# Kernel tuning notes

Hardware: AMD Instinct MI355X
Metric: run time of the kernel (lower is better)

The kernel has to match this reference:

```python
import jax, jax.numpy as jnp
import numpy as np
import math

B, T, V, D, H, L = 32, 512, 16, 256, 4, 2

def _ln(x, g, b, eps=1e-5):
    m = jnp.mean(x, -1, keepdims=True)
    v = jnp.mean((x - m) ** 2, -1, keepdims=True)
    return (x - m) * jax.lax.rsqrt(v + eps) * g + b

def _grn(x, w1, b1, w2, b2, g, bn, sw=None, sb=None):
    h = jax.nn.elu(x @ w1 + b1)
    h = h @ w2 + b2
    h1, h2 = jnp.split(h, 2, axis=-1)
    h = h1 * jax.nn.sigmoid(h2)
    skip = x if sw is None else x @ sw + sb
    return _ln(h + skip, g, bn)

def setup_inputs():
    ks = iter(jax.random.split(jax.random.key(0), 64))
    s = 0.02
    def w(*shape):
        return jax.random.normal(next(ks), shape, jnp.float32) * s
    return dict(
        x=jax.random.normal(next(ks), (B, T, V), jnp.float32),
        emb_w=w(V, D), emb_b=w(V, D),
        vg_fc1_w=w(V, D, D), vg_fc1_b=w(V, D), vg_fc2_w=w(V, D, 2 * D), vg_fc2_b=w(V, 2 * D),
        vg_ln_g=jnp.ones((V, D), jnp.float32), vg_ln_b=jnp.zeros((V, D), jnp.float32),
        sel_fc1_w=w(V * D, D), sel_fc1_b=w(D), sel_fc2_w=w(D, 2 * V), sel_fc2_b=w(2 * V),
        sel_skip_w=w(V * D, V), sel_skip_b=w(V),
        sel_ln_g=jnp.ones((V,), jnp.float32), sel_ln_b=jnp.zeros((V,), jnp.float32),
        lstm_wih=w(L, 4 * D, D), lstm_whh=w(L, 4 * D, D), lstm_bih=w(L, 4 * D), lstm_bhh=w(L, 4 * D),
        pl_fc1_w=w(D, D), pl_fc1_b=w(D), pl_fc2_w=w(D, 2 * D), pl_fc2_b=w(2 * D),
        pl_ln_g=jnp.ones((D,), jnp.float32), pl_ln_b=jnp.zeros((D,), jnp.float32),
        attn_in_w=w(3 * D, D), attn_in_b=w(3 * D), attn_out_w=w(D, D), attn_out_b=w(D),
        attn_ln_g=jnp.ones((D,), jnp.float32), attn_ln_b=jnp.zeros((D,), jnp.float32),
        pa_fc1_w=w(D, D), pa_fc1_b=w(D), pa_fc2_w=w(D, 2 * D), pa_fc2_b=w(2 * D),
        pa_ln_g=jnp.ones((D,), jnp.float32), pa_ln_b=jnp.zeros((D,), jnp.float32),
        fg_fc1_w=w(D, 4 * D), fg_fc1_b=w(4 * D), fg_fc2_w=w(4 * D, 2 * D), fg_fc2_b=w(2 * D),
        fg_ln_g=jnp.ones((D,), jnp.float32), fg_ln_b=jnp.zeros((D,), jnp.float32),
    )

def reference(x, emb_w, emb_b, vg_fc1_w, vg_fc1_b, vg_fc2_w, vg_fc2_b, vg_ln_g, vg_ln_b,
              sel_fc1_w, sel_fc1_b, sel_fc2_w, sel_fc2_b, sel_skip_w, sel_skip_b, sel_ln_g, sel_ln_b,
              lstm_wih, lstm_whh, lstm_bih, lstm_bhh,
              pl_fc1_w, pl_fc1_b, pl_fc2_w, pl_fc2_b, pl_ln_g, pl_ln_b,
              attn_in_w, attn_in_b, attn_out_w, attn_out_b, attn_ln_g, attn_ln_b,
              pa_fc1_w, pa_fc1_b, pa_fc2_w, pa_fc2_b, pa_ln_g, pa_ln_b,
              fg_fc1_w, fg_fc1_b, fg_fc2_w, fg_fc2_b, fg_ln_g, fg_ln_b):
    b, t, v = x.shape
    d = emb_w.shape[1]
    # per-feature Linear(1, d) fused into one broadcasted op: [B,T,V,D]
    embedded = x[..., None] * emb_w + emb_b
    # per-variable GRNs (no skip_fc since input==output), batched over V via einsum
    h = jax.nn.elu(jnp.einsum('btvd,vdh->btvh', embedded, vg_fc1_w) + vg_fc1_b)
    h = jnp.einsum('btvh,vho->btvo', h, vg_fc2_w) + vg_fc2_b
    h1, h2 = jnp.split(h, 2, axis=-1)
    var_out = _ln(h1 * jax.nn.sigmoid(h2) + embedded, vg_ln_g, vg_ln_b)  # [B,T,V,D]
    # selection GRN over flattened variables
    flat = embedded.reshape(b, t, v * d)
    sel = _grn(flat, sel_fc1_w, sel_fc1_b, sel_fc2_w, sel_fc2_b, sel_ln_g, sel_ln_b, sel_skip_w, sel_skip_b)
    weights = jax.nn.softmax(sel, axis=-1)  # [B,T,V]
    vsn_out = jnp.einsum('btvh,btv->bth', var_out, weights)  # [B,T,D]
    # stacked LSTM (torch gate order i,f,g,o); dropout inactive at eval
    h_seq = vsn_out
    for l in range(lstm_wih.shape[0]):
        xi = jnp.einsum('btd,gd->btg', h_seq, lstm_wih[l]) + lstm_bih[l] + lstm_bhh[l]
        whh = lstm_whh[l]
        def step(carry, xt):
            hp, cp = carry
            gates = xt + hp @ whh.T
            i, f, g, o = jnp.split(gates, 4, axis=-1)
            c = jax.nn.sigmoid(f) * cp + jax.nn.sigmoid(i) * jnp.tanh(g)
            hh = jax.nn.sigmoid(o) * jnp.tanh(c)
            return (hh, c), hh
        init = (jnp.zeros((b, d), x.dtype), jnp.zeros((b, d), x.dtype))
        _, hs = jax.lax.scan(step, init, jnp.swapaxes(xi, 0, 1))
        h_seq = jnp.swapaxes(hs, 0, 1)
    lstm_filtered = _grn(h_seq + vsn_out, pl_fc1_w, pl_fc1_b, pl_fc2_w, pl_fc2_b, pl_ln_g, pl_ln_b)
    # multihead self-attention
    qkv = lstm_filtered @ attn_in_w.T + attn_in_b
    q, k, vv = jnp.split(qkv, 3, axis=-1)
    hd = d // H
    def heads(z):
        return z.reshape(b, t, H, hd).transpose(0, 2, 1, 3)
    q, k, vv = heads(q), heads(k), heads(vv)
    scale = 1.0 / math.sqrt(hd)
    att = jax.nn.softmax(jnp.einsum('bhqd,bhkd->bhqk', q, k) * scale, axis=-1)
    o = jnp.einsum('bhqk,bhkd->bhqd', att, vv).transpose(0, 2, 1, 3).reshape(b, t, d)
    o = o @ attn_out_w.T + attn_out_b
    attn_out = _ln(o + lstm_filtered, attn_ln_g, attn_ln_b)
    attn_filtered = _grn(attn_out, pa_fc1_w, pa_fc1_b, pa_fc2_w, pa_fc2_b, pa_ln_g, pa_ln_b)
    out = _grn(attn_filtered, fg_fc1_w, fg_fc1_b, fg_fc2_w, fg_fc2_b, fg_ln_g, fg_ln_b)
    return out[:, -1, :], weights
```

## Files before the change

kernel.cpp:

```cpp
#include <hip/hip_runtime.h>
#include <hip/hip_bf16.h>
#include <hip/hip_fp8.h>
#include <math.h>


#define BT 16384
#define TT 512
#define BB 32
#define VV 16
#define DD 256

typedef unsigned short ushort;
typedef unsigned int uint;
typedef unsigned long ulong_;
typedef __attribute__((ext_vector_type(8))) short short8;
typedef __attribute__((ext_vector_type(8))) unsigned short ushort8v;
typedef __attribute__((ext_vector_type(4))) float floatx4;
typedef __attribute__((ext_vector_type(8))) int int8v;

#if __has_builtin(__builtin_amdgcn_cvt_pk_fp8_f32)
#define HW_FP8_CVT 1
#endif

__device__ __forceinline__ float sigmoidf_(float x) { return 1.f / (1.f + expf(-x)); }
__device__ __forceinline__ float eluf_(float x)     { return x > 0.f ? x : expm1f(x); }
__device__ __forceinline__ float fsig(float x) {
  return __builtin_amdgcn_rcpf(1.f + __expf(-x));
}
__device__ __forceinline__ float ftanh(float x) {
  float xc = fminf(fmaxf(x, -44.f), 44.f);
  float e = __expf(-2.f * xc);
  return (1.f - e) * __builtin_amdgcn_rcpf(1.f + e);
}
__device__ __forceinline__ ushort f2bf(float f) {
  unsigned int u = __float_as_uint(f);
  unsigned int r = u + 0x7fffu + ((u >> 16) & 1u);
  return (ushort)(r >> 16);
}
__device__ __forceinline__ float bf2f(ushort b) { return __uint_as_float(((unsigned int)b) << 16); }

__device__ __forceinline__ float2 bsum256x2(float a, float b, float* red8) {
  #pragma unroll
  for (int m = 32; m > 0; m >>= 1) { a += __shfl_xor(a, m, 64); b += __shfl_xor(b, m, 64); }
  int w = threadIdx.x >> 6;
  if ((threadIdx.x & 63) == 0) { red8[w * 2] = a; red8[w * 2 + 1] = b; }
  __syncthreads();
  float ra = red8[0] + red8[2] + red8[4] + red8[6];
  float rb = red8[1] + red8[3] + red8[5] + red8[7];
  __syncthreads();
  return make_float2(ra, rb);
}

__device__ __forceinline__ float block_sum256(float v, float* red) {
  int j = threadIdx.x;
  red[j] = v; __syncthreads();
  #pragma unroll
  for (int st = 128; st > 0; st >>= 1) {
    if (j < st) red[j] += red[j + st];
    __syncthreads();
  }
  float r = red[0];
  __syncthreads();
  return r;
}

__global__ void wtT_k(const float* __restrict__ src, ushort* __restrict__ dst,
                      int K, int N, long sStride, long dStride) {
  int b = blockIdx.z;
  src += (size_t)b * sStride; dst += (size_t)b * dStride;
  __shared__ float t[32][33];
  int k0 = blockIdx.y * 32, n0 = blockIdx.x * 32;
  int tx = threadIdx.x & 31, ty = threadIdx.x >> 5;
  #pragma unroll
  for (int i = 0; i < 32; i += 8) {
    int k = k0 + ty + i, n = n0 + tx;
    t[ty + i][tx] = (k < K && n < N) ? src[(size_t)k * N + n] : 0.f;
  }
  __syncthreads();
  #pragma unroll
  for (int i = 0; i < 32; i += 8) {
    int n = n0 + ty + i, k = k0 + tx;
    if (n < N && k < K) dst[(size_t)n * K + k] = f2bf(t[tx][ty + i]);
  }
}

__global__ void cvt_k(const float* __restrict__ src, ushort* __restrict__ dst, int n) {
  int i = blockIdx.x * 256 + threadIdx.x;
  if (i < n) dst[i] = f2bf(src[i]);
}

__global__ void redw_k(const float* __restrict__ W, int ldw,
                       const float* __restrict__ ew, const float* __restrict__ eb,
                       const float* __restrict__ bias, int biasPerV,
                       float* __restrict__ R, float* __restrict__ C, int N) {
  int v = blockIdx.x;
  int n = threadIdx.x;
  if (n >= N) return;
  const float* Wb = W + (size_t)v * 256 * ldw + n;
  const float* ewv = ew + v * 256;
  const float* ebv = eb + v * 256;
  float r = 0.f, c = 0.f;
  for (int j = 0; j < 256; j++) {
    float w = Wb[(size_t)j * ldw];
    r += ewv[j] * w;
    c += ebv[j] * w;
  }
  if (biasPerV) c += bias[v * 256 + n];
  R[v * N + n] = r;
  C[v * N + n] = c;
}

__global__ __launch_bounds__(256) void sel_h_k(const float* __restrict__ x,
                                               const float* __restrict__ R1,
                                               const float* __restrict__ C1,
                                               const float* __restrict__ b1,
                                               ushort* __restrict__ selH) {
  int m = blockIdx.x, n = threadIdx.x;
  __shared__ float xs[16];
  if (n < 16) xs[n] = x[m * 16 + n];
  __syncthreads();
  float a = b1[n];
  #pragma unroll
  for (int v = 0; v < 16; v++) a += xs[v] * R1[v * 256 + n] + C1[v * 256 + n];
  selH[(size_t)m * 256 + n] = f2bf(eluf_(a));
}

__global__ void sel_skip_k(const float* __restrict__ x,
                           const float* __restrict__ Rsk, const float* __restrict__ Csk,
                           const float* __restrict__ b, float* __restrict__ selSkip) {
  int gid = blockIdx.x * 256 + threadIdx.x;
  int m = gid >> 4, n = gid & 15;
  const float* xr = x + m * 16;
  float a = b[n];
  #pragma unroll
  for (int v = 0; v < 16; v++) a += xr[v] * Rsk[v * 16 + n] + Csk[v * 16 + n];
  selSkip[gid] = a;
}

__global__ void w2pack_k(const float* __restrict__ src, ushort* __restrict__ dst) {
  int z = blockIdx.z, kt = blockIdx.y, n0 = blockIdx.x * 64;
  __shared__ float t[32][65];
  for (int i = threadIdx.x; i < 2048; i += 256) {
    int r = i >> 6, c = i & 63;
    t[r][c] = src[(size_t)z * 131072 + (size_t)(kt * 32 + r) * 512 + n0 + c];
  }
  __syncthreads();
  for (int i = threadIdx.x; i < 2048; i += 256) {
    int c = i >> 5, kk = i & 31;
    dst[((size_t)(z * 8 + kt) * 512 + n0 + c) * 32 + kk] = f2bf(t[kk][c]);
  }
}

__global__ void whh_pack8_k(const float* __restrict__ whh, unsigned char* __restrict__ dst) {
  int gid = blockIdx.x * 256 + threadIdx.x;
  int layer = gid >> 13;
  int rem = gid & 8191;
  int lane = rem & 63;
  int f = (rem >> 6) & 15;
  int wave = rem >> 10;
  int kt2 = f & 1, ts = (f >> 1) & 1, g = f >> 2;
  int n = g * 256 + wave * 32 + ts * 16 + (lane & 15);
  int k0 = kt2 * 128 + (lane >> 4) * 32;
  const float* src = whh + (size_t)layer * 262144 + (size_t)n * 256 + k0;
  unsigned char* d = dst + (size_t)gid * 32;
  #pragma unroll
  for (int b = 0; b < 32; b++) {
    __hip_fp8_e4m3 q(src[b] * 64.f);
    d[b] = q.__x;
  }
}

__global__ __launch_bounds__(256, 1) void var_fused_k(
    const float* __restrict__ x,
    const ushort* __restrict__ w2p,
    const float* __restrict__ fc2b,
    const float* __restrict__ varR, const float* __restrict__ varC,
    const float* __restrict__ embw, const float* __restrict__ embb,
    const float* __restrict__ lng, const float* __restrict__ lnb,
    const float* __restrict__ wts,
    float* __restrict__ vsn) {
  int m0 = blockIdx.x * 64;
  int tid = threadIdx.x;
  int wave = tid >> 6, lane = tid & 63;
  int lm = lane & 15, lq = lane >> 4;
  __shared__ ushort As[64][40];
  __shared__ ushort Bs[512][40];
  __shared__ float xs[64][17];
  __shared__ float wss[64][17];
  for (int i = tid; i < 64 * 16; i += 256) {
    int m = i >> 4, v = i & 15;
    xs[m][v]  = x[(size_t)(m0 + m) * 16 + v];
    wss[m][v] = wts[(size_t)(m0 + m) * 16 + v];
  }
  floatx4 vac[16];
  #pragma unroll
  for (int nt = 0; nt < 16; nt++) vac[nt] = (floatx4)0.f;

  int am = tid & 63;
  int ak = (tid >> 6) * 8;
  ushort8v pf[8];
  {
    const ushort8v* s0 = (const ushort8v*)w2p + (size_t)tid * 8;
    #pragma unroll
    for (int q = 0; q < 8; q++) pf[q] = s0[q];
  }
  float4 rA0 = *(const float4*)&varR[ak];
  float4 rA1 = *(const float4*)&varR[ak + 4];
  float4 cA0 = *(const float4*)&varC[ak];
  float4 cA1 = *(const float4*)&varC[ak + 4];
  __syncthreads();

  for (int z = 0; z < 16; z++) {
    floatx4 acc[32];
    #pragma unroll
    for (int q = 0; q < 32; q++) acc[q] = (floatx4)0.f;
    float xv = xs[am][z];
    for (int kt = 0; kt < 8; kt++) {
      int bn = tid * 2;
      *(ushort8v*)&Bs[bn][0]      = pf[0];
      *(ushort8v*)&Bs[bn][8]      = pf[1];
      *(ushort8v*)&Bs[bn][16]     = pf[2];
      *(ushort8v*)&Bs[bn][24]     = pf[3];
      *(ushort8v*)&Bs[bn + 1][0]  = pf[4];
      *(ushort8v*)&Bs[bn + 1][8]  = pf[5];
      *(ushort8v*)&Bs[bn + 1][16] = pf[6];
      *(ushort8v*)&Bs[bn + 1][24] = pf[7];
      {
        float rr[8] = {rA0.x, rA0.y, rA0.z, rA0.w, rA1.x, rA1.y, rA1.z, rA1.w};
        float cc[8] = {cA0.x, cA0.y, cA0.z, cA0.w, cA1.x, cA1.y, cA1.z, cA1.w};
        ushort tmp[8];
        #pragma unroll
        for (int q = 0; q < 8; q++) tmp[q] = f2bf(eluf_(xv * rr[q] + cc[q]));
        *(ushort8v*)&As[am][ak] = *(ushort8v*)tmp;
      }
      int nz = (kt == 7) ? z + 1 : z;
      int nk = (kt == 7) ? 0 : kt + 1;
      if (nz < 16) {
        const ushort8v* sn = (const ushort8v*)w2p + (size_t)(nz * 8 + nk) * 2048 + (size_t)tid * 8;
        #pragma unroll
        for (int q = 0; q < 8; q++) pf[q] = sn[q];
        int rb = nz * 256 + nk * 32 + ak;
        rA0 = *(const float4*)&varR[rb]; rA1 = *(const float4*)&varR[rb + 4];
        cA0 = *(const float4*)&varC[rb]; cA1 = *(const float4*)&varC[rb + 4];
      }
      __syncthreads();
      short8 fa = *(const short8*)&As[wave * 16 + lm][lq * 8];
      #pragma unroll
      for (int nt = 0; nt < 32; nt++) {
        short8 fb = *(const short8*)&Bs[nt * 16 + lm][lq * 8];
        acc[nt] = __builtin_amdgcn_mfma_f32_16x16x32_bf16(fa, fb, acc[nt], 0, 0, 0);
      }
      __syncthreads();
    }
    int strip = wave * 16;
    float xz[4], wz[4];
    #pragma unroll
    for (int rg = 0; rg < 4; rg++) {
      int r4 = strip + lq * 4 + rg;
      xz[rg] = xs[r4][z];
      wz[rg] = wss[r4][z];
    }
    float sum[4] = {0.f, 0.f, 0.f, 0.f}, sq[4] = {0.f, 0.f, 0.f, 0.f};
    #pragma unroll
    for (int nt = 0; nt < 16; nt++) {
      int col = nt * 16 + lm;
      float b1 = fc2b[z * 512 + col];
      float b2 = fc2b[z * 512 + 256 + col];
      float ew = embw[z * 256 + col];
      float eb = embb[z * 256 + col];
      #pragma unroll
      for (int rg = 0; rg < 4; rg++) {
        float h1 = acc[nt][rg] + b1;
        float h2 = acc[nt + 16][rg] + b2;
        float s = h1 * fsig(h2) + (xz[rg] * ew + eb);
        acc[nt][rg] = s;
        sum[rg] += s; sq[rg] += s * s;
      }
    }
    #pragma unroll
    for (int rg = 0; rg < 4; rg++) {
      #pragma unroll
      for (int msk = 1; msk < 16; msk <<= 1) {
        sum[rg] += __shfl_xor(sum[rg], msk, 64);
        sq[rg]  += __shfl_xor(sq[rg],  msk, 64);
      }
    }
    float mean[4], inv[4];
    #pragma unroll
    for (int rg = 0; rg < 4; rg++) {
      mean[rg] = sum[rg] * (1.f / 256.f);
      float var = sq[rg] * (1.f / 256.f) - mean[rg] * mean[rg];
      inv[rg] = rsqrtf(var + 1e-5f);
    }
    #pragma unroll
    for (int nt = 0; nt < 16; nt++) {
      int col = nt * 16 + lm;
      float g = lng[z * 256 + col];
      float b = lnb[z * 256 + col];
      #pragma unroll
      for (int rg = 0; rg < 4; rg++) {
        float o = (acc[nt][rg] - mean[rg]) * inv[rg] * g + b;
        vac[nt][rg] += wz[rg] * o;
      }
    }
  }
  int strip = wave * 16;
  #pragma unroll
  for (int nt = 0; nt < 16; nt++) {
    #pragma unroll
    for (int rg = 0; rg < 4; rg++) {
      vsn[(size_t)(m0 + strip + lq * 4 + rg) * 256 + nt * 16 + lm] = vac[nt][rg];
    }
  }
}

template<int ADT, int ACT, int CDT>
__global__ __launch_bounds__(256) void mgemm_k(
    const void* __restrict__ Aall, int lda, long aStride,
    const ushort* __restrict__ Ball, long bStride,
    const float* __restrict__ biasAll, long biasStride,
    void* __restrict__ Call, int ldc, long cStride,
    int K, int Nvalid,
    const float* __restrict__ embw, const float* __restrict__ embb, int xbase) {
  int z = blockIdx.z;
  const ushort* B = Ball + (size_t)z * bStride;
  const float* bias = biasAll ? biasAll + (size_t)z * biasStride : nullptr;
  int m0 = blockIdx.y * 128, n0 = blockIdx.x * 128;
  __shared__ ushort As[128][40];
  __shared__ ushort Bs[128][40];
  int tid = threadIdx.x;
  int r = tid >> 1, half = tid & 1;
  int wave = tid >> 6, lane = tid & 63;
  int wm = (wave >> 1) * 64, wn = (wave & 1) * 64;
  int lm = lane & 15, lq = lane >> 4;
  floatx4 acc[4][4];
  #pragma unroll
  for (int i = 0; i < 4; i++)
    #pragma unroll
    for (int j = 0; j < 4; j++) acc[i][j] = (floatx4)0.f;

  for (int k0 = 0; k0 < K; k0 += 32) {
    int kk = k0 + half * 16;
    {
      int gm = m0 + r;
      ushort tmp[16];
      if (ADT == 0) {
        const float* Af = (const float*)Aall + (size_t)z * aStride + (size_t)gm * lda + kk;
        #pragma unroll
        for (int q = 0; q < 4; q++) {
          float4 f = ((const float4*)Af)[q];
          tmp[q * 4 + 0] = f2bf(f.x); tmp[q * 4 + 1] = f2bf(f.y);
          tmp[q * 4 + 2] = f2bf(f.z); tmp[q * 4 + 3] = f2bf(f.w);
        }
      } else if (ADT == 1) {
        const ushort* Ab = (const ushort*)Aall + (size_t)z * aStride + (size_t)gm * lda + kk;
        *(ushort8v*)&tmp[0] = *(const ushort8v*)(Ab);
        *(ushort8v*)&tmp[8] = *(const ushort8v*)(Ab + 8);
      } else {
        const float* A1 = (const float*)Aall + (size_t)z * aStride + (size_t)gm * lda + kk;
        const float* A2 = embw + (size_t)z * aStride + (size_t)gm * lda + kk;
        #pragma unroll
        for (int q = 0; q < 4; q++) {
          float4 f1 = ((const float4*)A1)[q];
          float4 f2 = ((const float4*)A2)[q];
          tmp[q * 4 + 0] = f2bf(f1.x + f2.x); tmp[q * 4 + 1] = f2bf(f1.y + f2.y);
          tmp[q * 4 + 2] = f2bf(f1.z + f2.z); tmp[q * 4 + 3] = f2bf(f1.w + f2.w);
        }
      }
      *(ushort8v*)&As[r][half * 16]     = *(ushort8v*)&tmp[0];
      *(ushort8v*)&As[r][half * 16 + 8] = *(ushort8v*)&tmp[8];
    }
    {
      int gn = n0 + r;
      ushort tmp[16];
      if (gn < Nvalid) {
        const ushort* Bp = B + (size_t)gn * K + kk;
        *(ushort8v*)&tmp[0] = *(const ushort8v*)(Bp);
        *(ushort8v*)&tmp[8] = *(const ushort8v*)(Bp + 8);
      } else {
        #pragma unroll
        for (int q = 0; q < 16; q++) tmp[q] = 0;
      }
      *(ushort8v*)&Bs[r][half * 16]     = *(ushort8v*)&tmp[0];
      *(ushort8v*)&Bs[r][half * 16 + 8] = *(ushort8v*)&tmp[8];
    }
    __syncthreads();
    short8 fa[4], fb[4];
    #pragma unroll
    for (int i = 0; i < 4; i++) fa[i] = *(const short8*)&As[wm + i * 16 + lm][lq * 8];
    #pragma unroll
    for (int j = 0; j < 4; j++) fb[j] = *(const short8*)&Bs[wn + j * 16 + lm][lq * 8];
    #pragma unroll
    for (int i = 0; i < 4; i++)
      #pragma unroll
      for (int j = 0; j < 4; j++)
        acc[i][j] = __builtin_amdgcn_mfma_f32_16x16x32_bf16(fa[i], fb[j], acc[i][j], 0, 0, 0);
    __syncthreads();
  }
  #pragma unroll
  for (int j = 0; j < 4; j++) {
    int gn = n0 + wn + j * 16 + lm;
    if (gn >= Nvalid) continue;
    float bv = bias ? bias[gn] : 0.f;
    #pragma unroll
    for (int i = 0; i < 4; i++) {
      #pragma unroll
      for (int rg = 0; rg < 4; rg++) {
        int gm = m0 + wm + i * 16 + lq * 4 + rg;
        float v = acc[i][j][rg] + bv;
        if (ACT == 1) v = eluf_(v);
        if (CDT == 0) ((float*)Call + (size_t)z * cStride)[(size_t)gm * ldc + gn] = v;
        else ((ushort*)Call + (size_t)z * cStride)[(size_t)gm * ldc + gn] = f2bf(v);
      }
    }
  }
}

__global__ void sel_finish_k(const float* __restrict__ selG, const float* __restrict__ selSkip,
                             const float* __restrict__ lng, const float* __restrict__ lnb,
                             float* __restrict__ wout, int M) {
  int m = blockIdx.x * 256 + threadIdx.x;
  if (m >= M) return;
  float s[16];
  float mean = 0.f;
  #pragma unroll
  for (int i = 0; i < 16; i++) {
    float h1 = selG[m * 32 + i], h2 = selG[m * 32 + 16 + i];
    float val = h1 * sigmoidf_(h2) + selSkip[m * 16 + i];
    s[i] = val; mean += val;
  }
  mean *= (1.f / 16.f);
  float var = 0.f;
  #pragma unroll
  for (int i = 0; i < 16; i++) { float d = s[i] - mean; var += d * d; }
  var *= (1.f / 16.f);
  float inv = rsqrtf(var + 1e-5f);
  float mx = -1e30f;
  #pragma unroll
  for (int i = 0; i < 16; i++) { s[i] = (s[i] - mean) * inv * lng[i] + lnb[i]; mx = fmaxf(mx, s[i]); }
  float sum = 0.f;
  #pragma unroll
  for (int i = 0; i < 16; i++) { s[i] = expf(s[i] - mx); sum += s[i]; }
  float isum = 1.f / sum;
  #pragma unroll
  for (int i = 0; i < 16; i++) wout[m * 16 + i] = s[i] * isum;
}

__global__ __launch_bounds__(256) void grn_epi_k(
    const ushort* __restrict__ G, const float* __restrict__ skipA,
    const float* __restrict__ skipB,
    const float* __restrict__ lng, const float* __restrict__ lnb,
    float* __restrict__ out) {
  int m = blockIdx.x, j = threadIdx.x;
  __shared__ float red8[8];
  float g1 = bf2f(G[(size_t)m * 512 + j]), g2 = bf2f(G[(size_t)m * 512 + 256 + j]);
  float sk = skipA[(size_t)m * 256 + j];
  if (skipB) sk += skipB[(size_t)m * 256 + j];
  float s = g1 * sigmoidf_(g2) + sk;
  float2 r = bsum256x2(s, s * s, red8);
  float mean = r.x * (1.f / 256.f);
  float var = r.y * (1.f / 256.f) - mean * mean;
  out[(size_t)m * 256 + j] = (s - mean) * rsqrtf(var + 1e-5f) * lng[j] + lnb[j];
}

__global__ void add2_k(const float* __restrict__ a, const float* __restrict__ b,
                       float* __restrict__ c, int n) {
  int i = blockIdx.x * 256 + threadIdx.x;
  if (i < n) c[i] = a[i] + b[i];
}

#define DESC (1.f / 1024.f)
#define H8S 272
__global__ __launch_bounds__(512, 2) void lstm_recur_k(
    const float* __restrict__ xi,
    const unsigned char* __restrict__ wpk,
    float* __restrict__ hout,
    int T) {
  int bb = blockIdx.x;
  int tid = threadIdx.x;
  int wave = tid >> 6, lane = tid & 63;
  int lm = lane & 15, lq = lane >> 4;
  __shared__ __align__(16) unsigned char h8[2][16 * H8S];
  for (int i = tid; i < 2 * 16 * H8S / 4; i += 512) ((uint*)h8)[i] = 0;

  int8v wr[16];
  {
    const int8v* wp = (const int8v*)wpk;
    #pragma unroll
    for (int f = 0; f < 16; f++) wr[f] = wp[(wave * 16 + f) * 64 + lane];
  }
  bool act = (lq == 0);
  int jj = wave * 32 + lm;
  const float* xg = xi + (size_t)bb * T * 1024;
  float xq[8], xn[8];
  if (act) {
    #pragma unroll
    for (int g = 0; g < 4; g++) {
      xq[2 * g]     = xg[g * 256 + jj];
      xq[2 * g + 1] = xg[g * 256 + jj + 16];
    }
  }
  float cst[2] = {0.f, 0.f};
  float hbf[2][8];
  int arow = lm * H8S + lq * 32;
  __syncthreads();

  for (int t = 0; t < T; t++) {
    int cur = t & 1, nxt = cur ^ 1;
    if (act && t + 1 < T) {
      const float* xp = xg + (size_t)(t + 1) * 1024;
      #pragma unroll
      for (int g = 0; g < 4; g++) {
        xn[2 * g]     = xp[g * 256 + jj];
        xn[2 * g + 1] = xp[g * 256 + jj + 16];
      }
    }
    int8v a[2];
    #pragma unroll
    for (int kt = 0; kt < 2; kt++)
      a[kt] = *(const int8v*)&h8[cur][arow + kt * 128];
    floatx4 acc[8];
    #pragma unroll
    for (int f = 0; f < 8; f++) acc[f] = (floatx4)0.f;
    #pragma unroll
    for (int kt = 0; kt < 2; kt++)
      #pragma unroll
      for (int f = 0; f < 8; f++)
        acc[f] = __builtin_amdgcn_mfma_scale_f32_16x16x128_f8f6f4(
            a[kt], wr[f * 2 + kt], acc[f], 0, 0, 0, 0x7f7f7f7f, 0, 0x7f7f7f7f);
    if (act) {
      int tb = t & 7;
      #pragma unroll
      for (int ts = 0; ts < 2; ts++) {
        float pi = acc[0 + ts][0] * DESC + xq[0 + ts];
        float pf = acc[2 + ts][0] * DESC + xq[2 + ts];
        float pg = acc[4 + ts][0] * DESC + xq[4 + ts];
        float po = acc[6 + ts][0] * DESC + xq[6 + ts];
        float c = fsig(pf) * cst[ts] + fsig(pi) * ftanh(pg);
        cst[ts] = c;
        hbf[ts][tb] = fsig(po) * ftanh(c);
      }
#ifdef HW_FP8_CVT
      int pk = __builtin_amdgcn_cvt_pk_fp8_f32(hbf[0][tb] * 16.f, hbf[1][tb] * 16.f, 0, false);
      h8[nxt][jj]      = (unsigned char)(pk & 0xff);
      h8[nxt][jj + 16] = (unsigned char)((pk >> 8) & 0xff);
#else
      __hip_fp8_e4m3 q0(hbf[0][tb] * 16.f), q1(hbf[1][tb] * 16.f);
      h8[nxt][jj]      = q0.__x;
      h8[nxt][jj + 16] = q1.__x;
#endif
      if (tb == 7) {
        #pragma unroll
        for (int q = 0; q < 8; q++) {
          size_t base = ((size_t)(bb * T + t - 7 + q)) * 256;
          hout[base + jj]      = hbf[0][q];
          hout[base + jj + 16] = hbf[1][q];
        }
      }
      #pragma unroll
      for (int g = 0; g < 8; g++) xq[g] = xn[g];
    }
    __syncthreads();
  }
}

__global__ __launch_bounds__(256) void attn_decode_k(const float* __restrict__ qkv,
                                                     float* __restrict__ o, int T) {
  int bh = blockIdx.x; int b = bh >> 2, h = bh & 3;
  int tid = threadIdx.x;
  __shared__ float q[64];
  __shared__ float p[512];
  __shared__ float red[256];
  if (tid < 64) q[tid] = qkv[((size_t)(b * T + T - 1)) * 768 + h * 64 + tid];
  __syncthreads();
  for (int t = tid; t < 512; t += 256) {
    const float* kv = qkv + ((size_t)(b * T + t)) * 768 + 256 + h * 64;
    float s = 0.f;
    #pragma unroll 16
    for (int d = 0; d < 64; d++) s += q[d] * kv[d];
    p[t] = s * 0.125f;
  }
  __syncthreads();
  red[tid] = fmaxf(p[tid], p[tid + 256]); __syncthreads();
  for (int st = 128; st > 0; st >>= 1) { if (tid < st) red[tid] = fmaxf(red[tid], red[tid + st]); __syncthreads(); }
  float mx = red[0]; __syncthreads();
  float e0 = expf(p[tid] - mx), e1 = expf(p[tid + 256] - mx);
  red[tid] = e0 + e1; __syncthreads();
  for (int st = 128; st > 0; st >>= 1) { if (tid < st) red[tid] += red[tid + st]; __syncthreads(); }
  float inv = 1.f / red[0];
  __syncthreads();
  p[tid] = e0; p[tid + 256] = e1;
  __syncthreads();
  int d = tid & 63, grp = tid >> 6;
  float acc = 0.f;
  for (int t = grp * 128; t < grp * 128 + 128; t++)
    acc += p[t] * qkv[((size_t)(b * T + t)) * 768 + 512 + h * 64 + d];
  red[tid] = acc; __syncthreads();
  if (grp == 0)
    o[(b * 4 + h) * 64 + d] = (red[tid] + red[tid + 64] + red[tid + 128] + red[tid + 192]) * inv;
}

__global__ __launch_bounds__(256) void attn_proj_ln_k(
    const float* __restrict__ attnO, const float* __restrict__ W, const float* __restrict__ bias,
    const float* __restrict__ lstmF, const float* __restrict__ lng, const float* __restrict__ lnb,
    float* __restrict__ out, int T) {
  int bb = blockIdx.x, j = threadIdx.x;
  __shared__ float a[256];
  __shared__ float red[256];
  a[j] = attnO[bb * 256 + j];
  __syncthreads();
  float acc = bias[j];
  const float* wr = W + (size_t)j * 256;
  #pragma unroll 8
  for (int k = 0; k < 256; k += 4) {
    float4 w4 = *(const float4*)(wr + k);
    acc += a[k] * w4.x + a[k + 1] * w4.y + a[k + 2] * w4.z + a[k + 3] * w4.w;
  }
  float s = acc + lstmF[((size_t)(bb * T + T - 1)) * 256 + j];
  float mean = block_sum256(s, red) * (1.f / 256.f);
  float d = s - mean;
  float var = block_sum256(d * d, red) * (1.f / 256.f);
  out[bb * 256 + j] = d * rsqrtf(var + 1e-5f) * lng[j] + lnb[j];
}

__global__ __launch_bounds__(256) void final_grns_k(
    const float* __restrict__ ain,
    const float* __restrict__ paw1, const float* __restrict__ pab1,
    const float* __restrict__ paw2, const float* __restrict__ pab2,
    const float* __restrict__ palg, const float* __restrict__ palb,
    const float* __restrict__ fgw1, const float* __restrict__ fgb1,
    const float* __restrict__ fgw2, const float* __restrict__ fgb2,
    const float* __restrict__ fglg, const float* __restrict__ fglb,
    float* __restrict__ out) {
  int bb = blockIdx.x, j = threadIdx.x;
  __shared__ float a[256];
  __shared__ float hbuf[1024];
  __shared__ float red[256];
  a[j] = ain[bb * 256 + j];
  __syncthreads();
  float acc = pab1[j];
  for (int k = 0; k < 256; k++) acc += a[k] * paw1[k * 256 + j];
  hbuf[j] = eluf_(acc);
  __syncthreads();
  float g1 = pab2[j], g2 = pab2[256 + j];
  for (int k = 0; k < 256; k++) { float hv = hbuf[k]; g1 += hv * paw2[k * 512 + j]; g2 += hv * paw2[k * 512 + 256 + j]; }
  float s = g1 * sigmoidf_(g2) + a[j];
  float mean = block_sum256(s, red) * (1.f / 256.f);
  float d = s - mean;
  float var = block_sum256(d * d, red) * (1.f / 256.f);
  float af = d * rsqrtf(var + 1e-5f) * palg[j] + palb[j];
  __syncthreads();
  a[j] = af;
  __syncthreads();
  float hh[4];
  #pragma unroll
  for (int q = 0; q < 4; q++) {
    int jj = j + q * 256;
    float ac = fgb1[jj];
    for (int k = 0; k < 256; k++) ac += a[k] * fgw1[k * 1024 + jj];
    hh[q] = eluf_(ac);
  }
  __syncthreads();
  #pragma unroll
  for (int q = 0; q < 4; q++) hbuf[j + q * 256] = hh[q];
  __syncthreads();
  float G1 = fgb2[j], G2 = fgb2[256 + j];
  for (int k = 0; k < 1024; k++) { float hv = hbuf[k]; G1 += hv * fgw2[k * 512 + j]; G2 += hv * fgw2[k * 512 + 256 + j]; }
  float s2 = G1 * sigmoidf_(G2) + a[j];
  mean = block_sum256(s2, red) * (1.f / 256.f);
  d = s2 - mean;
  var = block_sum256(d * d, red) * (1.f / 256.f);
  out[bb * 256 + j] = d * rsqrtf(var + 1e-5f) * fglg[j] + fglb[j];
}

extern "C" void kernel_launch(void* const* d_in, const int* in_sizes, int n_in,
                              void* d_out, int out_size, void* d_ws, size_t ws_size,
                              hipStream_t stream) {
  const float* x          = (const float*)d_in[0];
  const float* emb_w      = (const float*)d_in[1];
  const float* emb_b      = (const float*)d_in[2];
  const float* vg_fc1_w   = (const float*)d_in[3];
  const float* vg_fc1_b   = (const float*)d_in[4];
  const float* vg_fc2_w   = (const float*)d_in[5];
  const float* vg_fc2_b   = (const float*)d_in[6];
  const float* vg_ln_g    = (const float*)d_in[7];
  const float* vg_ln_b    = (const float*)d_in[8];
  const float* sel_fc1_w  = (const float*)d_in[9];
  const float* sel_fc1_b  = (const float*)d_in[10];
  const float* sel_fc2_w  = (const float*)d_in[11];
  const float* sel_fc2_b  = (const float*)d_in[12];
  const float* sel_skip_w = (const float*)d_in[13];
  const float* sel_skip_b = (const float*)d_in[14];
  const float* sel_ln_g   = (const float*)d_in[15];
  const float* sel_ln_b   = (const float*)d_in[16];
  const float* lstm_wih   = (const float*)d_in[17];
  const float* lstm_whh   = (const float*)d_in[18];
  const float* lstm_bih   = (const float*)d_in[19];
  const float* lstm_bhh   = (const float*)d_in[20];
  const float* pl_fc1_w   = (const float*)d_in[21];
  const float* pl_fc1_b   = (const float*)d_in[22];
  const float* pl_fc2_w   = (const float*)d_in[23];
  const float* pl_fc2_b   = (const float*)d_in[24];
  const float* pl_ln_g    = (const float*)d_in[25];
  const float* pl_ln_b    = (const float*)d_in[26];
  const float* attn_in_w  = (const float*)d_in[27];
  const float* attn_in_b  = (const float*)d_in[28];
  const float* attn_out_w = (const float*)d_in[29];
  const float* attn_out_b = (const float*)d_in[30];
  const float* attn_ln_g  = (const float*)d_in[31];
  const float* attn_ln_b  = (const float*)d_in[32];
  const float* pa_fc1_w   = (const float*)d_in[33];
  const float* pa_fc1_b   = (const float*)d_in[34];
  const float* pa_fc2_w   = (const float*)d_in[35];
  const float* pa_fc2_b   = (const float*)d_in[36];
  const float* pa_ln_g    = (const float*)d_in[37];
  const float* pa_ln_b    = (const float*)d_in[38];
  const float* fg_fc1_w   = (const float*)d_in[39];
  const float* fg_fc1_b   = (const float*)d_in[40];
  const float* fg_fc2_w   = (const float*)d_in[41];
  const float* fg_fc2_b   = (const float*)d_in[42];
  const float* fg_ln_g    = (const float*)d_in[43];
  const float* fg_ln_b    = (const float*)d_in[44];
  (void)in_sizes; (void)n_in; (void)out_size; (void)ws_size;

  float* out     = (float*)d_out;
  float* out_wts = out + BB * DD;

  char* p = (char*)d_ws;
  ushort* wt_sel_fc2  = (ushort*)p;                 p += 8192 * 2;
  ushort* wt_var_fc2p = (ushort*)p;                 p += 2097152 * 2;
  ushort* wt_wih      = (ushort*)p;                 p += 524288 * 2;
  unsigned char* wt_whh_pk8 = (unsigned char*)p;    p += 524288;
  ushort* wt_pl_fc1   = (ushort*)p;                 p += 65536 * 2;
  ushort* wt_pl_fc2   = (ushort*)p;                 p += 131072 * 2;
  ushort* wt_attn     = (ushort*)p;                 p += 196608 * 2;
  float*  selR        = (float*)p;                  p += 4096 * 4;
  float*  selC        = (float*)p;                  p += 4096 * 4;
  float*  varR        = (float*)p;                  p += 4096 * 4;
  float*  varC        = (float*)p;                  p += 4096 * 4;
  float*  skR         = (float*)p;                  p += 256 * 4;
  float*  skC         = (float*)p;                  p += 256 * 4;
  ushort* selH        = (ushort*)p;                 p += (size_t)BT * 256 * 2;
  float*  selSkip     = (float*)p;                  p += (size_t)BT * 16 * 4;
  float*  selG        = (float*)p;                  p += (size_t)BT * 32 * 4;
  float*  vsn         = (float*)p;                  p += (size_t)BT * 256 * 4;
  float*  hseq1       = (float*)p;                  p += (size_t)BT * 256 * 4;
  float*  hseq2       = (float*)p;                  p += (size_t)BT * 256 * 4;
  float*  cbias       = (float*)p;                  p += 4096 * 4;
  float*  attnO       = (float*)p;                  p += 8192 * 4;
  float*  attnLN      = (float*)p;                  p += 8192 * 4;
  char*   R           = p;
  float*  xi     = (float*)R;
  ushort* plH    = (ushort*)(R + (((size_t)16) << 20));
  ushort* plG    = (ushort*)(R + (((size_t)24) << 20));
  float*  lstmF  = (float*)(R + (((size_t)48) << 20));
  float*  qkv    = (float*)R;

  dim3 blk(256);

  wtT_k<<<dim3(1, 8, 1),    blk, 0, stream>>>(sel_fc2_w,  wt_sel_fc2,  256,  32,  0, 0);
  w2pack_k<<<dim3(8, 8, 16), blk, 0, stream>>>(vg_fc2_w, wt_var_fc2p);
  wtT_k<<<dim3(8, 8, 1),    blk, 0, stream>>>(pl_fc1_w,   wt_pl_fc1,   256,  256, 0, 0);
  wtT_k<<<dim3(16, 8, 1),   blk, 0, stream>>>(pl_fc2_w,   wt_pl_fc2,   256,  512, 0, 0);
  cvt_k<<<2048, blk, 0, stream>>>(lstm_wih,  wt_wih, 524288);
  whh_pack8_k<<<64, blk, 0, stream>>>(lstm_whh, wt_whh_pk8);
  cvt_k<<<768,  blk, 0, stream>>>(attn_in_w, wt_attn, 196608);
  add2_k<<<8, blk, 0, stream>>>(lstm_bih, lstm_bhh, cbias, 4096);
  redw_k<<<16, 256, 0, stream>>>(sel_fc1_w,  256, emb_w, emb_b, nullptr,   0, selR, selC, 256);
  redw_k<<<16, 256, 0, stream>>>(vg_fc1_w,   256, emb_w, emb_b, vg_fc1_b,  1, varR, varC, 256);
  redw_k<<<16, 64,  0, stream>>>(sel_skip_w, 16,  emb_w, emb_b, nullptr,   0, skR,  skC,  16);

  sel_h_k<<<BT, blk, 0, stream>>>(x, selR, selC, sel_fc1_b, selH);
  sel_skip_k<<<1024, blk, 0, stream>>>(x, skR, skC, sel_skip_b, selSkip);
  mgemm_k<1,0,0><<<dim3(1, 128, 1), blk, 0, stream>>>(selH, 256, 0, wt_sel_fc2, 0, sel_fc2_b, 0,
      selG, 32, 0, 256, 32, nullptr, nullptr, 0);
  sel_finish_k<<<64, blk, 0, stream>>>(selG, selSkip, sel_ln_g, sel_ln_b, out_wts, BT);

  var_fused_k<<<BT / 64, blk, 0, stream>>>(x, wt_var_fc2p, vg_fc2_b, varR, varC,
      emb_w, emb_b, vg_ln_g, vg_ln_b, out_wts, vsn);

  mgemm_k<0,0,0><<<dim3(8, 128, 1), blk, 0, stream>>>(vsn, 256, 0, wt_wih, 0, cbias, 0,
      xi, 1024, 0, 256, 1024, nullptr, nullptr, 0);
  lstm_recur_k<<<32, 512, 0, stream>>>(xi, wt_whh_pk8, hseq1, TT);
  mgemm_k<0,0,0><<<dim3(8, 128, 1), blk, 0, stream>>>(hseq1, 256, 0, wt_wih + 1024 * 256, 0,
      cbias + 1024, 0, xi, 1024, 0, 256, 1024, nullptr, nullptr, 0);
  lstm_recur_k<<<32, 512, 0, stream>>>(xi, wt_whh_pk8 + 262144, hseq2, TT);

  mgemm_k<3,1,1><<<dim3(2, 128, 1), blk, 0, stream>>>(hseq2, 256, 0, wt_pl_fc1, 0, pl_fc1_b, 0,
      plH, 256, 0, 256, 256, vsn, nullptr, 0);
  mgemm_k<1,0,1><<<dim3(4, 128, 1), blk, 0, stream>>>(plH, 256, 0, wt_pl_fc2, 0, pl_fc2_b, 0,
      plG, 512, 0, 256, 512, nullptr, nullptr, 0);
  grn_epi_k<<<BT, blk, 0, stream>>>(plG, hseq2, vsn, pl_ln_g, pl_ln_b, lstmF);

  mgemm_k<0,0,0><<<dim3(6, 128, 1), blk, 0, stream>>>(lstmF, 256, 0, wt_attn, 0, attn_in_b, 0,
      qkv, 768, 0, 256, 768, nullptr, nullptr, 0);
  attn_decode_k<<<BB * 4, blk, 0, stream>>>(qkv, attnO, TT);
  attn_proj_ln_k<<<BB, blk, 0, stream>>>(attnO, attn_out_w, attn_out_b, lstmF,
                                         attn_ln_g, attn_ln_b, attnLN, TT);

  final_grns_k<<<BB, blk, 0, stream>>>(attnLN,
      pa_fc1_w, pa_fc1_b, pa_fc2_w, pa_fc2_b, pa_ln_g, pa_ln_b,
      fg_fc1_w, fg_fc1_b, fg_fc2_w, fg_fc2_b, fg_ln_g, fg_ln_b,
      out);
}
```

Before: 2.032 ms.

## Compute Q only for last token; project only K,V over sequence

```diff
diff --git a/kernel.cpp b/kernel.cpp
--- a/kernel.cpp
+++ b/kernel.cpp
@@ -503,6 +503,7 @@
   float cst[2] = {0.f, 0.f};
   float hbf[2][8];
   int arow = lm * H8S + lq * 32;
+  const floatx4 z4 = (floatx4)0.f;
   __syncthreads();
 
   for (int t = 0; t < T; t++) {
@@ -521,13 +522,13 @@
       a[kt] = *(const int8v*)&h8[cur][arow + kt * 128];
     floatx4 acc[8];
     #pragma unroll
-    for (int f = 0; f < 8; f++) acc[f] = (floatx4)0.f;
-    #pragma unroll
-    for (int kt = 0; kt < 2; kt++)
-      #pragma unroll
-      for (int f = 0; f < 8; f++)
-        acc[f] = __builtin_amdgcn_mfma_scale_f32_16x16x128_f8f6f4(
-            a[kt], wr[f * 2 + kt], acc[f], 0, 0, 0, 0x7f7f7f7f, 0, 0x7f7f7f7f);
+    for (int f = 0; f < 8; f++)
+      acc[f] = __builtin_amdgcn_mfma_scale_f32_16x16x128_f8f6f4(
+          a[0], wr[f * 2 + 0], z4, 0, 0, 0, 0x7f7f7f7f, 0, 0x7f7f7f7f);
+    #pragma unroll
+    for (int f = 0; f < 8; f++)
+      acc[f] = __builtin_amdgcn_mfma_scale_f32_16x16x128_f8f6f4(
+          a[1], wr[f * 2 + 1], acc[f], 0, 0, 0, 0x7f7f7f7f, 0, 0x7f7f7f7f);
     if (act) {
       int tb = t & 7;
       #pragma unroll
@@ -564,20 +565,38 @@
   }
 }
 
-__global__ __launch_bounds__(256) void attn_decode_k(const float* __restrict__ qkv,
+__global__ __launch_bounds__(256) void attn_q_k(
+    const float* __restrict__ lstmF, const float* __restrict__ W,
+    const float* __restrict__ bias, float* __restrict__ qbuf, int T) {
+  int bb = blockIdx.x, n = threadIdx.x;
+  __shared__ float a[256];
+  a[n] = lstmF[((size_t)(bb * T + T - 1)) * 256 + n];
+  __syncthreads();
+  float acc = bias[n];
+  const float* wr = W + (size_t)n * 256;
+  #pragma unroll 8
+  for (int k = 0; k < 256; k += 4) {
+    float4 w4 = *(const float4*)(wr + k);
+    acc += a[k] * w4.x + a[k + 1] * w4.y + a[k + 2] * w4.z + a[k + 3] * w4.w;
+  }
+  qbuf[bb * 256 + n] = acc;
+}
+
+__global__ __launch_bounds__(256) void attn_decode_k(const float* __restrict__ qbuf,
+                                                     const float* __restrict__ kv,
                                                      float* __restrict__ o, int T) {
   int bh = blockIdx.x; int b = bh >> 2, h = bh & 3;
   int tid = threadIdx.x;
   __shared__ float q[64];
   __shared__ float p[512];
   __shared__ float red[256];
-  if (tid < 64) q[tid] = qkv[((size_t)(b * T + T - 1)) * 768 + h * 64 + tid];
+  if (tid < 64) q[tid] = qbuf[b * 256 + h * 64 + tid];
   __syncthreads();
   for (int t = tid; t < 512; t += 256) {
-    const float* kv = qkv + ((size_t)(b * T + t)) * 768 + 256 + h * 64;
+    const float* kp = kv + ((size_t)(b * T + t)) * 512 + h * 64;
     float s = 0.f;
     #pragma unroll 16
-    for (int d = 0; d < 64; d++) s += q[d] * kv[d];
+    for (int d = 0; d < 64; d++) s += q[d] * kp[d];
     p[t] = s * 0.125f;
   }
   __syncthreads();
@@ -594,7 +613,7 @@
   int d = tid & 63, grp = tid >> 6;
   float acc = 0.f;
   for (int t = grp * 128; t < grp * 128 + 128; t++)
-    acc += p[t] * qkv[((size_t)(b * T + t)) * 768 + 512 + h * 64 + d];
+    acc += p[t] * kv[((size_t)(b * T + t)) * 512 + 256 + h * 64 + d];
   red[tid] = acc; __syncthreads();
   if (grp == 0)
     o[(b * 4 + h) * 64 + d] = (red[tid] + red[tid + 64] + red[tid + 128] + red[tid + 192]) * inv;
@@ -749,12 +768,13 @@
   float*  cbias       = (float*)p;                  p += 4096 * 4;
   float*  attnO       = (float*)p;                  p += 8192 * 4;
   float*  attnLN      = (float*)p;                  p += 8192 * 4;
+  float*  qbuf        = (float*)p;                  p += 8192 * 4;
   char*   R           = p;
   float*  xi     = (float*)R;
   ushort* plH    = (ushort*)(R + (((size_t)16) << 20));
   ushort* plG    = (ushort*)(R + (((size_t)24) << 20));
   float*  lstmF  = (float*)(R + (((size_t)48) << 20));
-  float*  qkv    = (float*)R;
+  float*  kv     = (float*)R;
 
   dim3 blk(256);
 
@@ -792,9 +812,11 @@
       plG, 512, 0, 256, 512, nullptr, nullptr, 0);
   grn_epi_k<<<BT, blk, 0, stream>>>(plG, hseq2, vsn, pl_ln_g, pl_ln_b, lstmF);
 
-  mgemm_k<0,0,0><<<dim3(6, 128, 1), blk, 0, stream>>>(lstmF, 256, 0, wt_attn, 0, attn_in_b, 0,
-      qkv, 768, 0, 256, 768, nullptr, nullptr, 0);
-  attn_decode_k<<<BB * 4, blk, 0, stream>>>(qkv, attnO, TT);
+  mgemm_k<0,0,0><<<dim3(4, 128, 1), blk, 0, stream>>>(lstmF, 256, 0,
+      wt_attn + (size_t)256 * 256, 0, attn_in_b + 256, 0,
+      kv, 512, 0, 256, 512, nullptr, nullptr, 0);
+  attn_q_k<<<BB, blk, 0, stream>>>(lstmF, attn_in_w, attn_in_b, qbuf, TT);
+  attn_decode_k<<<BB * 4, blk, 0, stream>>>(qbuf, kv, attnO, TT);
   attn_proj_ln_k<<<BB, blk, 0, stream>>>(attnO, attn_out_w, attn_out_b, lstmF,
                                          attn_ln_g, attn_ln_b, attnLN, TT);
 
```

Measured after the change: 2.058 ms. No clear change (+1.3%).
